# Optimization experiments

Measured on AMD Instinct MI355X. Metric: run time of the kernel, lower is better.

## Reference

```python
import jax, jax.numpy as jnp
import numpy as np
import math

N_CELLS = 16384
INPUT_DIM = 512
HIDDEN = 512


def build_neighbors(n):
    n_bits = max(1, int(math.ceil(math.log2(n))))
    idx = np.arange(n)
    flips = [idx ^ (1 << b) for b in range(n_bits)]
    ring = [(idx + 1) % n, (idx - 1) % n]
    allnb = np.stack(flips + ring, axis=1)
    # dedupe per row; for power-of-2 n every row has exactly n_bits+1 uniques
    rows = [sorted(set(r.tolist())) for r in allnb]
    return np.asarray(rows, dtype=np.int32)


def setup_inputs() -> dict:
    key = jax.random.key(0)
    ks = jax.random.split(key, 12)
    n, d, h = N_CELLS, INPUT_DIM, HIDDEN
    amp = jax.random.uniform(ks[0], (n, h)) * 0.5 + 0.5
    phase = jax.random.normal(ks[1], (n, h)) * 0.3 + (2 * math.pi * jnp.arange(n) / n)[:, None]
    return {
        "x": jax.random.normal(ks[2], (1, d), dtype=jnp.float32),
        "pump_W": jax.random.normal(ks[3], (n, d), dtype=jnp.float32) / np.sqrt(d),
        "pump_b": jax.random.normal(ks[4], (n,), dtype=jnp.float32) * 0.01,
        "dec_W": jax.random.normal(ks[5], (d, 2 * h), dtype=jnp.float32) / np.sqrt(2 * h),
        "dec_b": jax.random.normal(ks[6], (d,), dtype=jnp.float32) * 0.01,
        "cs_re": (amp * jnp.cos(phase)).astype(jnp.float32),
        "cs_im": (amp * jnp.sin(phase)).astype(jnp.float32),
        "excited": jax.random.uniform(ks[7], (n,)) * 0.6,  # some cells above 0.5 threshold
        "phase_vel": jax.random.normal(ks[8], (n, h), dtype=jnp.float32) * 0.05,
        "cav_re": jax.random.normal(ks[9], (h,), dtype=jnp.float32) * 0.01,
        "cav_im": jax.random.normal(ks[10], (h,), dtype=jnp.float32) * 0.01,
        "neighbors": jnp.asarray(build_neighbors(n)),
    }


def reference(x, pump_W, pump_b, dec_W, dec_b, cs_re, cs_im, excited, phase_vel, cav_re, cav_im, neighbors):
    states = (cs_re + 1j * cs_im).astype(jnp.complex64)          # [n,h]
    cavity = (cav_re + 1j * cav_im).astype(jnp.complex64)        # [h]

    # pump + excited fraction update
    pump = jax.nn.sigmoid(x @ pump_W.T + pump_b)[0]              # [n]
    excited = jnp.clip(excited * 0.95 + pump * 0.05, 0.0, 1.0)

    # free phase rotation: polar(1, 0.1*phase_vel)
    states = states * jnp.exp(1j * (phase_vel * 0.1)).astype(jnp.complex64)

    # neighbor phase coupling (hypercube + ring, k=15 neighbors each)
    ang = jnp.angle(states)                                      # [n,h]
    nb_states = states[neighbors]                                # [n,k,h]
    coupling = jnp.cos(ang[:, None, :] - ang[neighbors])         # [n,k,h]
    interference = 0.1 * jnp.sum(coupling * nb_states, axis=1)   # [n,h]
    k = neighbors.shape[1]
    new_states = 0.7 * states + 0.3 * interference / k

    # lasing: population inversion threshold
    lasing = excited > 0.5                                       # [n]
    n_lasing = jnp.sum(lasing)
    maskf = lasing.astype(jnp.float32)[:, None]
    # emission uses pre-phase-lock states (torch copies lasing_cells first)
    emission = jnp.sum(new_states * maskf, axis=0) / jnp.maximum(n_lasing, 1).astype(jnp.float32)
    cavity_new = jnp.where(n_lasing > 0, 0.8 * cavity + 0.2 * emission, cavity)

    # phase-lock lasing cells to (old) cavity phase
    cavity_phase = jnp.angle(cavity)                             # old cavity
    new_ang = jnp.angle(new_states)
    locked = 0.3 * cavity_phase[None, :] + 0.7 * new_ang
    locked_states = jnp.abs(new_states) * jnp.exp(1j * locked)
    new_states = jnp.where(lasing[:, None], locked_states.astype(jnp.complex64), new_states)
    excited = jnp.where(lasing, excited * 0.9, excited * 0.98)

    # cavity feedback (updated cavity) + amplitude renorm
    new_states = new_states + 0.05 * cavity_new[None, :]
    amp = jnp.abs(new_states)
    amp = amp / (jnp.max(amp, axis=-1, keepdims=True) + 1e-8)
    final_states = (amp * jnp.exp(1j * jnp.angle(new_states))).astype(jnp.complex64)

    # decode cavity mode
    out_real = jnp.concatenate([cavity_new.real, cavity_new.imag])[None, :].astype(jnp.float32)  # [1,2h]
    pred = out_real @ dec_W.T + dec_b                            # [1, input_dim]
    tension = jnp.var(jnp.abs(final_states))
    return pred, tension
```

## Files before the change

### kernel.cpp

```cpp
#include <hip/hip_runtime.h>
#include <hip/hip_fp16.h>
#include <math.h>

#define N_CELLS 16384
#define HID 512
#define IND 512

#define ROT_BLOCKS  2048
#define PUMP_BLOCKS 4096

#define CPB 16
#define CELL_BLOCKS (N_CELLS / CPB)
#define PRED_BLOCKS 128

#define CNT_OFF   0
#define EMIS_OFF  128
#define CAV_OFF   4352
#define LAS_OFF   16384
#define VPART_OFF (LAS_OFF + N_CELLS*4)
#define ROT_OFF   (1<<20)
#define NST_OFF   (ROT_OFF + (size_t)N_CELLS*HID*4)

typedef unsigned int u32;

__device__ inline __half2 u2h(u32 u) { union { u32 u; __half2 h; } x; x.u = u; return x.h; }
__device__ inline u32 h2u(__half2 h) { union { u32 u; __half2 h; } x; x.h = h; return x.u; }
__device__ inline u32 packh2(float re, float im) { return h2u(__floats2half2_rn(re, im)); }
__device__ inline float2 unph2(u32 u) { __half2 h = u2h(u); return make_float2(__low2float(h), __high2float(h)); }

#if __has_builtin(__builtin_amdgcn_fdot2)
typedef _Float16 hv2 __attribute__((ext_vector_type(2)));
__device__ inline float dot2u(u32 a, u32 b) {
    union { u32 u; hv2 h; } x, y; x.u = a; y.u = b;
    return __builtin_amdgcn_fdot2(x.h, y.h, 0.f, false);
}
#else
__device__ inline float dot2u(u32 a, u32 b) {
    float2 af = unph2(a), bf = unph2(b);
    return fmaf(af.x, bf.x, af.y * bf.y);
}
#endif

__device__ inline void accnb(__half2& acc, u32 y, u32 q) {
    float d = dot2u(y, q);
    acc = __hfma2(__float2half2_rn(d), u2h(q), acc);
}

__device__ inline u32 fincell(u32 y, __half2 acc, int las, float& emR, float& emI) {
    float2 yf = unph2(y);
    float a  = fmaf(yf.x, yf.x, yf.y * yf.y);
    float rs = rsqrtf(a);
    float sq = a * rs;
    float2 af = make_float2(__low2float(acc), __high2float(acc));
    float nr = 0.7f * sq * yf.x + 0.002f * rs * af.x;
    float ni = 0.7f * sq * yf.y + 0.002f * rs * af.y;
    if (las) { emR += nr; emI += ni; }
    return packh2(nr, ni);
}

__device__ inline u32 rot1(float re, float im, float w) {
    float sc = rsqrtf(sqrtf(fmaf(re, re, im * im)));
    float s, c;
    __sincosf(0.1f * w, &s, &c);
    return packh2((re * c - im * s) * sc, (re * s + im * c) * sc);
}

__device__ inline float dot4(float4 a, float4 b) {
    return a.x * b.x + a.y * b.y + a.z * b.z + a.w * b.w;
}

__global__ __launch_bounds__(256, 2) void k_front(const float* __restrict__ cr,
        const float* __restrict__ ci, const float* __restrict__ pv,
        u32* __restrict__ yt,
        const float* __restrict__ x, const float* __restrict__ pW,
        const float* __restrict__ pb, const float* __restrict__ excited,
        int* __restrict__ lasing, int* __restrict__ cnt) {
    int b = blockIdx.x, tid = threadIdx.x;
    if (b < ROT_BLOCKS) {
        __shared__ u32 tile[64 * 65];
        int cb = b >> 3, hb = b & 7;
        const float4* cr4 = (const float4*)cr;
        const float4* ci4 = (const float4*)ci;
        const float4* pv4 = (const float4*)pv;
        float4 A[4], Bv[4], Wv[4];
        int row[4], c4[4];
#pragma unroll
        for (int j = 0; j < 4; ++j) {
            int idx = tid + 256 * j;
            row[j] = idx >> 4; c4[j] = idx & 15;
            size_t g = (size_t)(cb * 64 + row[j]) * 128 + hb * 16 + c4[j];
            A[j] = cr4[g]; Bv[j] = ci4[g]; Wv[j] = pv4[g];
        }
#pragma unroll
        for (int j = 0; j < 4; ++j) {
            u32* dst = &tile[row[j] * 65 + (c4[j] << 2)];
            dst[0] = rot1(A[j].x, Bv[j].x, Wv[j].x);
            dst[1] = rot1(A[j].y, Bv[j].y, Wv[j].y);
            dst[2] = rot1(A[j].z, Bv[j].z, Wv[j].z);
            dst[3] = rot1(A[j].w, Bv[j].w, Wv[j].w);
        }
        if (b == 0 && tid == 0) { cnt[0] = 0; cnt[1] = 0; }
        __syncthreads();
        uint4 v[4];
#pragma unroll
        for (int j = 0; j < 4; ++j) {
            int idx = tid + 256 * j;
            int chr = idx >> 4, q = idx & 15;
            v[j].x = tile[(q * 4 + 0) * 65 + chr];
            v[j].y = tile[(q * 4 + 1) * 65 + chr];
            v[j].z = tile[(q * 4 + 2) * 65 + chr];
            v[j].w = tile[(q * 4 + 3) * 65 + chr];
        }
#pragma unroll
        for (int j = 0; j < 4; ++j) {
            int idx = tid + 256 * j;
            int chr = idx >> 4, q = idx & 15;
            ((uint4*)(yt + (size_t)(hb * 64 + chr) * N_CELLS + cb * 64))[q] = v[j];
        }
    } else {
        int gtid = (b - ROT_BLOCKS) * 256 + tid;
        int cell = gtid >> 6, lane = gtid & 63;
        const float4* w4 = (const float4*)(pW + (size_t)cell * IND);
        const float4* x4 = (const float4*)x;
        float4 wa0 = w4[lane], wa1 = w4[lane + 64];
        float4 xb0 = x4[lane], xb1 = x4[lane + 64];
        float acc = dot4(wa0, xb0) + dot4(wa1, xb1);
#pragma unroll
        for (int o = 32; o; o >>= 1) acc += __shfl_xor(acc, o, 64);
        if (lane == 0) {
            float p = 1.f / (1.f + expf(-(acc + pb[cell])));
            float e = excited[cell] * 0.95f + p * 0.05f;
            e = fminf(fmaxf(e, 0.f), 1.f);
            lasing[cell] = (e > 0.5f) ? 1 : 0;
        }
    }
}

__global__ __launch_bounds__(256, 2) void k_coup(const u32* __restrict__ yt,
                                                 const int* __restrict__ lasv,
                                                 u32* __restrict__ nstT,
                                                 float2* __restrict__ emisT,
                                                 const float* __restrict__ cavr,
                                                 const float* __restrict__ cavi,
                                                 float* __restrict__ cavws,
                                                 int* __restrict__ cnt) {
    __shared__ __align__(16) u32 col[N_CELLS];
    int ch = blockIdx.x, tid = threadIdx.x;
    const uint4* src = (const uint4*)(yt + (size_t)ch * N_CELLS);
    uint4* cdst = (uint4*)col;
    {
        uint4 st[8];
#pragma unroll
        for (int k = 0; k < 8; ++k) st[k] = src[tid + 256 * k];
#pragma unroll
        for (int k = 0; k < 8; ++k) cdst[tid + 256 * k] = st[k];
#pragma unroll
        for (int k = 0; k < 8; ++k) st[k] = src[tid + 256 * (k + 8)];
#pragma unroll
        for (int k = 0; k < 8; ++k) cdst[tid + 256 * (k + 8)] = st[k];
    }
    __syncthreads();

    float emR = 0.f, emI = 0.f;
    int nlo = 0;
    uint4* outp = (uint4*)(nstT + (size_t)ch * N_CELLS);
    const int4* l4 = (const int4*)lasv;
    int4 lv_next = l4[tid];
#pragma unroll 2
    for (int j = 0; j < 16; ++j) {
        int s = tid + 256 * j;
        int4 lv = lv_next;
        if (j < 15) lv_next = l4[s + 256];
        int c = s << 2;
        uint4 sq = *(const uint4*)&col[c];
        __half2 z = __floats2half2_rn(0.f, 0.f);
        __half2 a0 = z, a1 = z, a2 = z, a3 = z;
#pragma unroll
        for (int bb = 2; bb < 14; ++bb) {
            uint4 q = *(const uint4*)&col[c ^ (1 << bb)];
            accnb(a0, sq.x, q.x);
            accnb(a1, sq.y, q.y);
            accnb(a2, sq.z, q.z);
            accnb(a3, sq.w, q.w);
        }
        u32 qm = col[(c - 1) & (N_CELLS - 1)];
        u32 qp = col[(c + 4) & (N_CELLS - 1)];
        accnb(a0, sq.x, sq.y); accnb(a0, sq.x, sq.z); accnb(a0, sq.x, qm);
        accnb(a1, sq.y, sq.x); accnb(a1, sq.y, sq.w); accnb(a1, sq.y, sq.z);
        accnb(a2, sq.z, sq.w); accnb(a2, sq.z, sq.x); accnb(a2, sq.z, sq.y);
        accnb(a3, sq.w, sq.z); accnb(a3, sq.w, sq.y); accnb(a3, sq.w, qp);
        nlo += lv.x + lv.y + lv.z + lv.w;
        uint4 ov;
        ov.x = fincell(sq.x, a0, lv.x, emR, emI);
        ov.y = fincell(sq.y, a1, lv.y, emR, emI);
        ov.z = fincell(sq.z, a2, lv.z, emR, emI);
        ov.w = fincell(sq.w, a3, lv.w, emR, emI);
        outp[s] = ov;
    }
    __syncthreads();
#pragma unroll
    for (int o = 32; o; o >>= 1) {
        emR += __shfl_xor(emR, o, 64);
        emI += __shfl_xor(emI, o, 64);
        nlo += __shfl_xor(nlo, o, 64);
    }
    float* scr = (float*)col;
    int* iscr = (int*)col;
    int wid = tid >> 6, lane = tid & 63;
    if (lane == 0) { scr[wid] = emR; scr[4 + wid] = emI; iscr[8 + wid] = nlo; }
    __syncthreads();
    if (tid == 0) {
        emisT[ch] = make_float2(scr[0] + scr[1] + scr[2] + scr[3],
                                scr[4] + scr[5] + scr[6] + scr[7]);
        __threadfence();
        int old = atomicAdd(cnt, 1);
        iscr[12] = (old == HID - 1) ? 1 : 0;
    }
    __syncthreads();
    if (iscr[12]) {
        __threadfence();
        int nl = iscr[8] + iscr[9] + iscr[10] + iscr[11];
        float inv = (nl > 0) ? 0.2f / (float)nl : 0.f;
#pragma unroll
        for (int k2 = 0; k2 < 2; ++k2) {
            int i = tid + 256 * k2;
            float crv = cavr[i], civ = cavi[i];
            float2 e = emisT[i];
            cavws[i]        = (nl > 0) ? 0.8f * crv + e.x * inv : crv;
            cavws[512 + i]  = (nl > 0) ? 0.8f * civ + e.y * inv : civ;
            cavws[1024 + i] = atan2f(civ, crv);
        }
    }
}

__global__ __launch_bounds__(256, 2) void k_finall(const u32* __restrict__ nstT,
        const int* __restrict__ lasv, const float* __restrict__ cavws,
        const float* __restrict__ dW, const float* __restrict__ db,
        float2* __restrict__ vpart, int* __restrict__ cnt2,
        float* __restrict__ out) {
    int b = blockIdx.x, t = threadIdx.x;
    int wid = t >> 6, lane = t & 63;
    if (b < CELL_BLOCKS) {
        __shared__ __align__(16) u32 tile[CPB * HID];
        __shared__ __align__(16) float scav[1536];
        __shared__ float w1[4], w2[4];
        __shared__ int slast;
        __shared__ double l1s[4], l2s[4];

        int c0 = b * CPB;
        uint4 ld[8]; int chv[8], qv[8];
#pragma unroll
        for (int j = 0; j < 8; ++j) {
            int idx = t + 256 * j;
            chv[j] = idx >> 2; qv[j] = idx & 3;
            ld[j] = ((const uint4*)(nstT + (size_t)chv[j] * N_CELLS + c0))[qv[j]];
        }
        const float4* c4p = (const float4*)cavws;
#pragma unroll
        for (int k2 = 0; k2 < 2; ++k2) {
            int i = t + 256 * k2;
            if (i < 384) ((float4*)scav)[i] = c4p[i];
        }
#pragma unroll
        for (int j = 0; j < 8; ++j) {
#pragma unroll
            for (int e = 0; e < 4; ++e) {
                int cell = qv[j] * 4 + e;
                int sw = chv[j] ^ (((e ^ qv[j]) & 1) << 4);
                tile[cell * HID + sw] = ((const u32*)&ld[j])[e];
            }
        }
        __syncthreads();

        int cell = t >> 4, kk = t & 15;
        int lasc = lasv[c0 + cell];
        int swb = ((cell ^ (cell >> 2)) & 1) << 4;
        const u32* trow = &tile[cell * HID];
        float sa = 0.f, sa2 = 0.f, mx = 0.f;
#pragma unroll 8
        for (int i = 0; i < 32; ++i) {
            int ch = kk + 16 * i;
            float2 vf = unph2(trow[ch ^ swb]);
            float vx = vf.x, vy = vf.y;
            if (lasc) {
                float r = sqrtf(fmaf(vx, vx, vy * vy));
                float lk = 0.3f * scav[1024 + ch] + 0.7f * atan2f(vy, vx);
                float sn, cs;
                __sincosf(lk, &sn, &cs);
                vx = r * cs; vy = r * sn;
            }
            vx += 0.05f * scav[ch];
            vy += 0.05f * scav[512 + ch];
            float a2v = fmaf(vx, vx, vy * vy);
            float a = sqrtf(a2v);
            sa += a; sa2 += a2v; mx = fmaxf(mx, a);
        }
#pragma unroll
        for (int o = 1; o < 16; o <<= 1) {
            sa += __shfl_xor(sa, o, 64);
            sa2 += __shfl_xor(sa2, o, 64);
            mx = fmaxf(mx, __shfl_xor(mx, o, 64));
        }
        float invm = 1.f / (mx + 1e-8f);
        float s1 = sa * invm, s2 = sa2 * invm * invm;
        s1 += __shfl_xor(s1, 16, 64); s2 += __shfl_xor(s2, 16, 64);
        s1 += __shfl_xor(s1, 32, 64); s2 += __shfl_xor(s2, 32, 64);
        if (lane == 0) { w1[wid] = s1; w2[wid] = s2; }
        __syncthreads();
        if (t == 0) {
            vpart[b] = make_float2(w1[0] + w1[1] + w1[2] + w1[3],
                                   w2[0] + w2[1] + w2[2] + w2[3]);
            __threadfence();
            int old = atomicAdd(cnt2, 1);
            slast = (old == CELL_BLOCKS - 1) ? 1 : 0;
        }
        __syncthreads();
        if (slast) {
            __threadfence();
            double d1 = (double)vpart[t].x + (double)vpart[t + 256].x
                      + (double)vpart[t + 512].x + (double)vpart[t + 768].x;
            double d2 = (double)vpart[t].y + (double)vpart[t + 256].y
                      + (double)vpart[t + 512].y + (double)vpart[t + 768].y;
#pragma unroll
            for (int o = 32; o; o >>= 1) { d1 += __shfl_xor(d1, o, 64); d2 += __shfl_xor(d2, o, 64); }
            if (lane == 0) { l1s[wid] = d1; l2s[wid] = d2; }
            __syncthreads();
            if (t == 0) {
                double t1 = l1s[0] + l1s[1] + l1s[2] + l1s[3];
                double t2 = l2s[0] + l2s[1] + l2s[2] + l2s[3];
                double nn = (double)N_CELLS * (double)HID;
                double mean = t1 / nn;
                out[IND] = (float)(t2 / nn - mean * mean);
            }
        }
    } else {
        int j = (b - CELL_BLOCKS) * 4 + wid;
        const float4* w4 = (const float4*)(dW + (size_t)j * (2 * HID));
        const float4* o4 = (const float4*)cavws;
        float a2 = 0.f;
#pragma unroll
        for (int tt = 0; tt < 4; ++tt) {
            float4 a = w4[lane + 64 * tt];
            float4 bx = o4[lane + 64 * tt];
            a2 += a.x * bx.x + a.y * bx.y + a.z * bx.z + a.w * bx.w;
        }
#pragma unroll
        for (int o = 32; o; o >>= 1) a2 += __shfl_xor(a2, o, 64);
        if (lane == 0) out[j] = a2 + db[j];
    }
}

extern "C" void kernel_launch(void* const* d_in, const int* in_sizes, int n_in,
                              void* d_out, int out_size, void* d_ws, size_t ws_size,
                              hipStream_t stream) {
    const float* x       = (const float*)d_in[0];
    const float* pump_W  = (const float*)d_in[1];
    const float* pump_b  = (const float*)d_in[2];
    const float* dec_W   = (const float*)d_in[3];
    const float* dec_b   = (const float*)d_in[4];
    const float* cs_re   = (const float*)d_in[5];
    const float* cs_im   = (const float*)d_in[6];
    const float* excited = (const float*)d_in[7];
    const float* pvel    = (const float*)d_in[8];
    const float* cav_re  = (const float*)d_in[9];
    const float* cav_im  = (const float*)d_in[10];

    float* out = (float*)d_out;
    char* ws = (char*)d_ws;
    int*    cnt   = (int*)(ws + CNT_OFF);
    float2* emisT = (float2*)(ws + EMIS_OFF);
    float*  cavws = (float*)(ws + CAV_OFF);
    int*    lasv  = (int*)(ws + LAS_OFF);
    float2* vpart = (float2*)(ws + VPART_OFF);
    u32*    yt    = (u32*)(ws + ROT_OFF);
    u32*    nstT  = (u32*)(ws + NST_OFF);

    k_front<<<ROT_BLOCKS + PUMP_BLOCKS, 256, 0, stream>>>(
        cs_re, cs_im, pvel, yt, x, pump_W, pump_b, excited, lasv, cnt);
    k_coup<<<HID, 256, 0, stream>>>(yt, lasv, nstT, emisT, cav_re, cav_im, cavws, cnt);
    k_finall<<<CELL_BLOCKS + PRED_BLOCKS, 256, 0, stream>>>(
        nstT, lasv, cavws, dec_W, dec_b, vpart, cnt + 1, out);
}
```

Baseline: 261.9 us.

## Pack lasing flags into bitmask and widen coupling blocks to 1024 threads

Lasing flags are now stored as a bitmask built with ballot and atomicOr, instead of an int array, which shrinks the flag reads in the coupling and final kernels. The pump dot product now uses 16 lanes per cell with 8 float4 loads each, so fewer pump blocks are launched. The coupling kernel moves to 1024-thread blocks with a 16-wave reduction, and sched_barriers separate the loads from the compute. A memset now zeroes the counters and bitmask, which adds one small launch.

```diff
diff --git a/kernel.cpp b/kernel.cpp
--- a/kernel.cpp
+++ b/kernel.cpp
@@ -7,17 +7,17 @@
 #define IND 512
 
 #define ROT_BLOCKS  2048
-#define PUMP_BLOCKS 4096
+#define PUMP_BLOCKS 1024
 
 #define CPB 16
 #define CELL_BLOCKS (N_CELLS / CPB)
 #define PRED_BLOCKS 128
 
 #define CNT_OFF   0
-#define EMIS_OFF  128
-#define CAV_OFF   4352
-#define LAS_OFF   16384
-#define VPART_OFF (LAS_OFF + N_CELLS*4)
+#define LASB_OFF  1024
+#define EMIS_OFF  8192
+#define CAV_OFF   16384
+#define VPART_OFF 32768
 #define ROT_OFF   (1<<20)
 #define NST_OFF   (ROT_OFF + (size_t)N_CELLS*HID*4)
 
@@ -69,12 +69,12 @@
     return a.x * b.x + a.y * b.y + a.z * b.z + a.w * b.w;
 }
 
-__global__ __launch_bounds__(256, 2) void k_front(const float* __restrict__ cr,
+__global__ __launch_bounds__(256, 3) void k_front(const float* __restrict__ cr,
         const float* __restrict__ ci, const float* __restrict__ pv,
         u32* __restrict__ yt,
         const float* __restrict__ x, const float* __restrict__ pW,
         const float* __restrict__ pb, const float* __restrict__ excited,
-        int* __restrict__ lasing, int* __restrict__ cnt) {
+        u32* __restrict__ lasb) {
     int b = blockIdx.x, tid = threadIdx.x;
     if (b < ROT_BLOCKS) {
         __shared__ u32 tile[64 * 65];
@@ -91,6 +91,7 @@
             size_t g = (size_t)(cb * 64 + row[j]) * 128 + hb * 16 + c4[j];
             A[j] = cr4[g]; Bv[j] = ci4[g]; Wv[j] = pv4[g];
         }
+        __builtin_amdgcn_sched_barrier(0);
 #pragma unroll
         for (int j = 0; j < 4; ++j) {
             u32* dst = &tile[row[j] * 65 + (c4[j] << 2)];
@@ -99,7 +100,6 @@
             dst[2] = rot1(A[j].z, Bv[j].z, Wv[j].z);
             dst[3] = rot1(A[j].w, Bv[j].w, Wv[j].w);
         }
-        if (b == 0 && tid == 0) { cnt[0] = 0; cnt[1] = 0; }
         __syncthreads();
         uint4 v[4];
 #pragma unroll
@@ -118,59 +118,66 @@
             ((uint4*)(yt + (size_t)(hb * 64 + chr) * N_CELLS + cb * 64))[q] = v[j];
         }
     } else {
-        int gtid = (b - ROT_BLOCKS) * 256 + tid;
-        int cell = gtid >> 6, lane = gtid & 63;
+        int c0 = (b - ROT_BLOCKS) * 16;
+        int cell = c0 + (tid >> 4);
+        int l16 = tid & 15;
+        int lane = tid & 63;
         const float4* w4 = (const float4*)(pW + (size_t)cell * IND);
         const float4* x4 = (const float4*)x;
-        float4 wa0 = w4[lane], wa1 = w4[lane + 64];
-        float4 xb0 = x4[lane], xb1 = x4[lane + 64];
-        float acc = dot4(wa0, xb0) + dot4(wa1, xb1);
-#pragma unroll
-        for (int o = 32; o; o >>= 1) acc += __shfl_xor(acc, o, 64);
-        if (lane == 0) {
+        float4 wv[8];
+#pragma unroll
+        for (int k = 0; k < 8; ++k) wv[k] = w4[l16 + 16 * k];
+        __builtin_amdgcn_sched_barrier(0);
+        float acc = 0.f;
+#pragma unroll
+        for (int k = 0; k < 8; ++k) acc += dot4(wv[k], x4[l16 + 16 * k]);
+#pragma unroll
+        for (int o = 1; o < 16; o <<= 1) acc += __shfl_xor(acc, o, 64);
+        int flag = 0;
+        if (l16 == 0) {
             float p = 1.f / (1.f + expf(-(acc + pb[cell])));
             float e = excited[cell] * 0.95f + p * 0.05f;
             e = fminf(fmaxf(e, 0.f), 1.f);
-            lasing[cell] = (e > 0.5f) ? 1 : 0;
-        }
-    }
-}
-
-__global__ __launch_bounds__(256, 2) void k_coup(const u32* __restrict__ yt,
-                                                 const int* __restrict__ lasv,
-                                                 u32* __restrict__ nstT,
-                                                 float2* __restrict__ emisT,
-                                                 const float* __restrict__ cavr,
-                                                 const float* __restrict__ cavi,
-                                                 float* __restrict__ cavws,
-                                                 int* __restrict__ cnt) {
+            flag = (e > 0.5f) ? 1 : 0;
+        }
+        unsigned long long bal = __ballot(flag);
+        if (lane == 0) {
+            u32 val = (u32)(bal & 1) | ((u32)(bal >> 16) & 1) << 1
+                    | ((u32)(bal >> 32) & 1) << 2 | ((u32)(bal >> 48) & 1) << 3;
+            atomicOr(&lasb[cell >> 5], val << (cell & 31));
+        }
+    }
+}
+
+__global__ __launch_bounds__(1024, 8) void k_coup(const u32* __restrict__ yt,
+                                                  const u32* __restrict__ lasb,
+                                                  u32* __restrict__ nstT,
+                                                  float2* __restrict__ emisT,
+                                                  const float* __restrict__ cavr,
+                                                  const float* __restrict__ cavi,
+                                                  float* __restrict__ cavws,
+                                                  int* __restrict__ cnt) {
     __shared__ __align__(16) u32 col[N_CELLS];
     int ch = blockIdx.x, tid = threadIdx.x;
     const uint4* src = (const uint4*)(yt + (size_t)ch * N_CELLS);
     uint4* cdst = (uint4*)col;
     {
-        uint4 st[8];
-#pragma unroll
-        for (int k = 0; k < 8; ++k) st[k] = src[tid + 256 * k];
-#pragma unroll
-        for (int k = 0; k < 8; ++k) cdst[tid + 256 * k] = st[k];
-#pragma unroll
-        for (int k = 0; k < 8; ++k) st[k] = src[tid + 256 * (k + 8)];
-#pragma unroll
-        for (int k = 0; k < 8; ++k) cdst[tid + 256 * (k + 8)] = st[k];
+        uint4 st[4];
+#pragma unroll
+        for (int k = 0; k < 4; ++k) st[k] = src[tid + 1024 * k];
+        __builtin_amdgcn_sched_barrier(0);
+#pragma unroll
+        for (int k = 0; k < 4; ++k) cdst[tid + 1024 * k] = st[k];
     }
     __syncthreads();
 
     float emR = 0.f, emI = 0.f;
     int nlo = 0;
     uint4* outp = (uint4*)(nstT + (size_t)ch * N_CELLS);
-    const int4* l4 = (const int4*)lasv;
-    int4 lv_next = l4[tid];
 #pragma unroll 2
-    for (int j = 0; j < 16; ++j) {
-        int s = tid + 256 * j;
-        int4 lv = lv_next;
-        if (j < 15) lv_next = l4[s + 256];
+    for (int j = 0; j < 4; ++j) {
+        int s = tid + 1024 * j;
+        u32 f = (lasb[s >> 3] >> ((s & 7) * 4)) & 0xF;
         int c = s << 2;
         uint4 sq = *(const uint4*)&col[c];
         __half2 z = __floats2half2_rn(0.f, 0.f);
@@ -189,12 +196,12 @@
         accnb(a1, sq.y, sq.x); accnb(a1, sq.y, sq.w); accnb(a1, sq.y, sq.z);
         accnb(a2, sq.z, sq.w); accnb(a2, sq.z, sq.x); accnb(a2, sq.z, sq.y);
         accnb(a3, sq.w, sq.z); accnb(a3, sq.w, sq.y); accnb(a3, sq.w, qp);
-        nlo += lv.x + lv.y + lv.z + lv.w;
+        nlo += __popc(f);
         uint4 ov;
-        ov.x = fincell(sq.x, a0, lv.x, emR, emI);
-        ov.y = fincell(sq.y, a1, lv.y, emR, emI);
-        ov.z = fincell(sq.z, a2, lv.z, emR, emI);
-        ov.w = fincell(sq.w, a3, lv.w, emR, emI);
+        ov.x = fincell(sq.x, a0, f & 1, emR, emI);
+        ov.y = fincell(sq.y, a1, f & 2, emR, emI);
+        ov.z = fincell(sq.z, a2, f & 4, emR, emI);
+        ov.w = fincell(sq.w, a3, f & 8, emR, emI);
         outp[s] = ov;
     }
     __syncthreads();
@@ -207,23 +214,25 @@
     float* scr = (float*)col;
     int* iscr = (int*)col;
     int wid = tid >> 6, lane = tid & 63;
-    if (lane == 0) { scr[wid] = emR; scr[4 + wid] = emI; iscr[8 + wid] = nlo; }
+    if (lane == 0) { scr[wid] = emR; scr[16 + wid] = emI; iscr[32 + wid] = nlo; }
     __syncthreads();
     if (tid == 0) {
-        emisT[ch] = make_float2(scr[0] + scr[1] + scr[2] + scr[3],
-                                scr[4] + scr[5] + scr[6] + scr[7]);
+        float sr = 0.f, si = 0.f; int sn = 0;
+#pragma unroll
+        for (int k = 0; k < 16; ++k) { sr += scr[k]; si += scr[16 + k]; sn += iscr[32 + k]; }
+        emisT[ch] = make_float2(sr, si);
+        iscr[48] = sn;
         __threadfence();
         int old = atomicAdd(cnt, 1);
-        iscr[12] = (old == HID - 1) ? 1 : 0;
+        iscr[49] = (old == HID - 1) ? 1 : 0;
     }
     __syncthreads();
-    if (iscr[12]) {
+    if (iscr[49]) {
         __threadfence();
-        int nl = iscr[8] + iscr[9] + iscr[10] + iscr[11];
+        int nl = iscr[48];
         float inv = (nl > 0) ? 0.2f / (float)nl : 0.f;
-#pragma unroll
-        for (int k2 = 0; k2 < 2; ++k2) {
-            int i = tid + 256 * k2;
+        if (tid < 512) {
+            int i = tid;
             float crv = cavr[i], civ = cavi[i];
             float2 e = emisT[i];
             cavws[i]        = (nl > 0) ? 0.8f * crv + e.x * inv : crv;
@@ -234,7 +243,7 @@
 }
 
 __global__ __launch_bounds__(256, 2) void k_finall(const u32* __restrict__ nstT,
-        const int* __restrict__ lasv, const float* __restrict__ cavws,
+        const u32* __restrict__ lasb, const float* __restrict__ cavws,
         const float* __restrict__ dW, const float* __restrict__ db,
         float2* __restrict__ vpart, int* __restrict__ cnt2,
         float* __restrict__ out) {
@@ -261,6 +270,7 @@
             int i = t + 256 * k2;
             if (i < 384) ((float4*)scav)[i] = c4p[i];
         }
+        __builtin_amdgcn_sched_barrier(0);
 #pragma unroll
         for (int j = 0; j < 8; ++j) {
 #pragma unroll
@@ -273,7 +283,8 @@
         __syncthreads();
 
         int cell = t >> 4, kk = t & 15;
-        int lasc = lasv[c0 + cell];
+        int cg = c0 + cell;
+        int lasc = (lasb[cg >> 5] >> (cg & 31)) & 1;
         int swb = ((cell ^ (cell >> 2)) & 1) << 4;
         const u32* trow = &tile[cell * HID];
         float sa = 0.f, sa2 = 0.f, mx = 0.f;
@@ -368,16 +379,17 @@
     float* out = (float*)d_out;
     char* ws = (char*)d_ws;
     int*    cnt   = (int*)(ws + CNT_OFF);
+    u32*    lasb  = (u32*)(ws + LASB_OFF);
     float2* emisT = (float2*)(ws + EMIS_OFF);
     float*  cavws = (float*)(ws + CAV_OFF);
-    int*    lasv  = (int*)(ws + LAS_OFF);
     float2* vpart = (float2*)(ws + VPART_OFF);
     u32*    yt    = (u32*)(ws + ROT_OFF);
     u32*    nstT  = (u32*)(ws + NST_OFF);
 
+    hipMemsetAsync(ws, 0, 4096, stream);
     k_front<<<ROT_BLOCKS + PUMP_BLOCKS, 256, 0, stream>>>(
-        cs_re, cs_im, pvel, yt, x, pump_W, pump_b, excited, lasv, cnt);
-    k_coup<<<HID, 256, 0, stream>>>(yt, lasv, nstT, emisT, cav_re, cav_im, cavws, cnt);
+        cs_re, cs_im, pvel, yt, x, pump_W, pump_b, excited, lasb);
+    k_coup<<<HID, 1024, 0, stream>>>(yt, lasb, nstT, emisT, cav_re, cav_im, cavws, cnt);
     k_finall<<<CELL_BLOCKS + PRED_BLOCKS, 256, 0, stream>>>(
-        nstT, lasv, cavws, dec_W, dec_b, vpart, cnt + 1, out);
-}
+        nstT, lasb, cavws, dec_W, dec_b, vpart, cnt + 1, out);
+}
```

Result: no change. 264.5 us (+1.0%).
